# Kernel tuning notes

Measured on AMD Instinct MI355X. Metric: run time of the kernel, lower is better.

## Reference

```python
import jax, jax.numpy as jnp
import numpy as np

V, D, B, S, T, MAXLEN = 32000, 256, 4, 512, 256, 512


def _gru(x, Wih, Whh, bih, bhh):
    """torch-style GRU over x:[B,L,Din] -> [B,L,D]. Weight rows ordered [r,z,n]."""
    Dh = Whh.shape[1]
    xW = x @ Wih.T + bih  # [B,L,3D] precompute input projections

    def step(h, xw):
        hW = h @ Whh.T + bhh
        xr, xz, xn = jnp.split(xw, 3, axis=-1)
        hr, hz, hn = jnp.split(hW, 3, axis=-1)
        r = jax.nn.sigmoid(xr + hr)
        z = jax.nn.sigmoid(xz + hz)
        n = jnp.tanh(xn + r * hn)
        h = (1.0 - z) * n + z * h
        return h, h

    h0 = jnp.zeros((x.shape[0], Dh), x.dtype)
    _, ys = jax.lax.scan(step, h0, jnp.swapaxes(xW, 0, 1))
    return jnp.swapaxes(ys, 0, 1)


def setup_inputs() -> dict:
    key = jax.random.key(0)
    ks = jax.random.split(key, 24)

    def n(k, shape, scale=0.02):
        return (jax.random.normal(k, shape, jnp.float32) * scale).astype(jnp.float32)

    inp = {
        "src": jax.random.randint(ks[0], (B, S), 0, V),
        "tgt": jax.random.randint(ks[1], (B, T), 0, V),
        "emb": n(ks[2], (V, D)),
        "pos": n(ks[3], (MAXLEN, D)),
        # encoder forward direction
        "ef_wih": n(ks[4], (3 * D, D)), "ef_whh": n(ks[5], (3 * D, D)),
        "ef_bih": n(ks[6], (3 * D,)), "ef_bhh": n(ks[7], (3 * D,)),
        # encoder backward direction
        "eb_wih": n(ks[8], (3 * D, D)), "eb_whh": n(ks[9], (3 * D, D)),
        "eb_bih": n(ks[10], (3 * D,)), "eb_bhh": n(ks[11], (3 * D,)),
        # decoder
        "d_wih": n(ks[12], (3 * D, D)), "d_whh": n(ks[13], (3 * D, D)),
        "d_bih": n(ks[14], (3 * D,)), "d_bhh": n(ks[15], (3 * D,)),
        "Wq": n(ks[16], (D, D)),
        "Wk": n(ks[17], (D, 2 * D)),
        "Wgen": n(ks[18], (V, 3 * D)), "bgen": n(ks[19], (V,)),
        "Wgate": n(ks[20], (1, 3 * D)), "bgate": n(ks[21], (1,)),
    }
    return inp


def reference(src, tgt, emb, pos,
              ef_wih, ef_whh, ef_bih, ef_bhh,
              eb_wih, eb_whh, eb_bih, eb_bhh,
              d_wih, d_whh, d_bih, d_bhh,
              Wq, Wk, Wgen, bgen, Wgate, bgate):
    b, s = src.shape
    t = tgt.shape[1]
    d = emb.shape[1]
    v = emb.shape[0]

    src_emb = emb[src] + pos[:s][None]          # [B,S,D]
    enc_f = _gru(src_emb, ef_wih, ef_whh, ef_bih, ef_bhh)
    enc_b = _gru(src_emb[:, ::-1], eb_wih, eb_whh, eb_bih, eb_bhh)[:, ::-1]
    enc_out = jnp.concatenate([enc_f, enc_b], axis=-1)  # [B,S,2D]

    tgt_emb = emb[tgt] + pos[:t][None]
    dec_out = _gru(tgt_emb, d_wih, d_whh, d_bih, d_bhh)  # [B,T,D]

    Q = dec_out @ Wq.T                           # [B,T,D]
    K = enc_out @ Wk.T                           # [B,S,D]
    scores = jnp.einsum('btd,bsd->bts', Q, K) / jnp.sqrt(jnp.asarray(d, jnp.float32))
    pos_probs = jax.nn.softmax(scores, axis=-1)  # [B,T,S]

    # copy distribution: scatter attention mass into vocab buckets (== one_hot bmm)
    P_copy = jnp.zeros((b, t, v), pos_probs.dtype).at[
        jnp.arange(b)[:, None, None],
        jnp.arange(t)[None, :, None],
        src[:, None, :],
    ].add(pos_probs)

    ctx_f = jnp.einsum('bts,bsd->btd', pos_probs, enc_f)
    ctx_b = jnp.einsum('bts,bsd->btd', pos_probs, enc_b)
    combined = jnp.concatenate([dec_out, ctx_f, ctx_b], axis=-1)  # [B,T,3D]

    P_gen = jax.nn.softmax(combined @ Wgen.T + bgen, axis=-1)     # [B,T,V]
    gate = jax.nn.sigmoid(combined @ Wgate.T + bgate)             # [B,T,1]
    return gate * P_gen + (1.0 - gate) * P_copy
```

## Files before the change

### kernel.cpp

```cpp
#include <hip/hip_runtime.h>
#include <hip/hip_bf16.h>
#include <math.h>

#define VV   32000
#define DIM  256
#define BB   4
#define SS   512
#define TT   256
#define D2   512
#define D3   768

typedef __attribute__((ext_vector_type(8))) short s16x8;
typedef __attribute__((ext_vector_type(4))) float f32x4;

__device__ __forceinline__ float sigmoidf_(float x) { return 1.0f / (1.0f + __expf(-x)); }
__device__ __forceinline__ float tanhf_(float x) {
    float e2 = __expf(2.0f * x);
    return (e2 - 1.0f) / (e2 + 1.0f);
}
__device__ __forceinline__ short f2bf(float f) {
    unsigned u = __float_as_uint(f);
    u += 0x7FFFu + ((u >> 16) & 1u);
    return (short)(u >> 16);
}

__global__ __launch_bounds__(256) void k_embed(const int* __restrict__ src,
                                               const int* __restrict__ tgt,
                                               const float* __restrict__ emb,
                                               const float* __restrict__ pos,
                                               float* __restrict__ src_emb,
                                               float* __restrict__ tgt_emb) {
    int i = blockIdx.x * 256 + threadIdx.x;
    const int nS = BB * SS * DIM;
    if (i < nS) {
        int d = i & (DIM - 1);
        int s = (i >> 8) & (SS - 1);
        int b = i >> 17;
        src_emb[i] = emb[(size_t)src[b * SS + s] * DIM + d] + pos[s * DIM + d];
    } else {
        int j = i - nS;
        int d = j & (DIM - 1);
        int t = (j >> 8) & (TT - 1);
        int b = j >> 16;
        tgt_emb[j] = emb[(size_t)tgt[b * TT + t] * DIM + d] + pos[t * DIM + d];
    }
}

#define BMM 128
#define BNN 128
#define BKK 8

__global__ __launch_bounds__(256) void k_gemm(const float* __restrict__ A, int lda,
                                              const float* __restrict__ Bt, int ldb,
                                              const float* __restrict__ bias,
                                              float* __restrict__ C, int ldc) {
    __shared__ float As[BKK][BMM + 4];
    __shared__ float Bs[BKK][BNN + 4];
    const int K = lda;
    int tid = threadIdx.x;
    int tx = tid & 15, ty = tid >> 4;
    int brow = blockIdx.y * BMM, bcol = blockIdx.x * BNN;
    float acc[8][8];
#pragma unroll
    for (int i = 0; i < 8; i++)
#pragma unroll
        for (int j = 0; j < 8; j++) acc[i][j] = 0.0f;

    int lr = tid >> 1;
    int lk = (tid & 1) * 4;
    for (int k0 = 0; k0 < K; k0 += BKK) {
        float4 a4 = *(const float4*)&A[(size_t)(brow + lr) * lda + k0 + lk];
        float4 b4 = *(const float4*)&Bt[(size_t)(bcol + lr) * ldb + k0 + lk];
        As[lk + 0][lr] = a4.x; As[lk + 1][lr] = a4.y; As[lk + 2][lr] = a4.z; As[lk + 3][lr] = a4.w;
        Bs[lk + 0][lr] = b4.x; Bs[lk + 1][lr] = b4.y; Bs[lk + 2][lr] = b4.z; Bs[lk + 3][lr] = b4.w;
        __syncthreads();
#pragma unroll
        for (int kk = 0; kk < BKK; kk++) {
            float4 a0 = *(const float4*)&As[kk][ty * 8];
            float4 a1 = *(const float4*)&As[kk][ty * 8 + 4];
            float4 b0 = *(const float4*)&Bs[kk][tx * 8];
            float4 b1 = *(const float4*)&Bs[kk][tx * 8 + 4];
            float av[8] = {a0.x, a0.y, a0.z, a0.w, a1.x, a1.y, a1.z, a1.w};
            float bv[8] = {b0.x, b0.y, b0.z, b0.w, b1.x, b1.y, b1.z, b1.w};
#pragma unroll
            for (int i = 0; i < 8; i++)
#pragma unroll
                for (int j = 0; j < 8; j++) acc[i][j] += av[i] * bv[j];
        }
        __syncthreads();
    }

    float bv0[8];
#pragma unroll
    for (int j = 0; j < 8; j++) bv0[j] = bias ? bias[bcol + tx * 8 + j] : 0.0f;

#pragma unroll
    for (int i = 0; i < 8; i++) {
        size_t row = brow + ty * 8 + i;
        float4 c0 = make_float4(acc[i][0] + bv0[0], acc[i][1] + bv0[1],
                                acc[i][2] + bv0[2], acc[i][3] + bv0[3]);
        float4 c1 = make_float4(acc[i][4] + bv0[4], acc[i][5] + bv0[5],
                                acc[i][6] + bv0[6], acc[i][7] + bv0[7]);
        *(float4*)&C[row * ldc + bcol + tx * 8] = c0;
        *(float4*)&C[row * ldc + bcol + tx * 8 + 4] = c1;
    }
}

__global__ __launch_bounds__(512, 2) void k_gru(const float* __restrict__ ef_x,
                                                const float* __restrict__ eb_x,
                                                const float* __restrict__ d_x,
                                                const float* __restrict__ ef_whh, const float* __restrict__ ef_bhh,
                                                const float* __restrict__ eb_whh, const float* __restrict__ eb_bhh,
                                                const float* __restrict__ d_whh, const float* __restrict__ d_bhh,
                                                float* __restrict__ enc_out,
                                                float* __restrict__ dec_out) {
    __shared__ __align__(16) short hb[2][4 * 256];

    int tid = threadIdx.x;
    int dir = blockIdx.x;
    const float *xw, *Whh, *bhh;
    int L;
    if (dir == 0)      { xw = ef_x; Whh = ef_whh; bhh = ef_bhh; L = SS; }
    else if (dir == 1) { xw = eb_x; Whh = eb_whh; bhh = eb_bhh; L = SS; }
    else               { xw = d_x;  Whh = d_whh;  bhh = d_bhh;  L = TT; }

    const int wv = tid >> 6;
    const int lane = tid & 63;
    const int jj = lane & 15;
    const int hi = lane >> 4;
    const int b = hi;

    if (tid < 256) {
        f32x4 z = {0.f, 0.f, 0.f, 0.f};
        *(f32x4*)((char*)hb + tid * 16) = z;
    }

    s16x8 wf[3][2][8];
#pragma unroll
    for (int g = 0; g < 3; ++g)
#pragma unroll
        for (int t = 0; t < 2; ++t) {
            const int nrow = g * 256 + wv * 32 + t * 16 + jj;
            const float* wp = Whh + (size_t)nrow * 256 + hi * 8;
#pragma unroll
            for (int sk = 0; sk < 8; ++sk) {
                float4 w0 = *(const float4*)(wp + sk * 32);
                float4 w1 = *(const float4*)(wp + sk * 32 + 4);
                s16x8 v;
                v[0] = f2bf(w0.x); v[1] = f2bf(w0.y); v[2] = f2bf(w0.z); v[3] = f2bf(w0.w);
                v[4] = f2bf(w1.x); v[5] = f2bf(w1.y); v[6] = f2bf(w1.z); v[7] = f2bf(w1.w);
                wf[g][t][sk] = v;
            }
        }

    const int j0 = wv * 32 + jj, j1 = j0 + 16;
    const float br0 = bhh[j0], bz0 = bhh[256 + j0], bn0 = bhh[512 + j0];
    const float br1 = bhh[j1], bz1 = bhh[256 + j1], bn1 = bhh[512 + j1];

    const int arow = jj >> 2;
    const int abase = arow * 512 + hi * 16;
    const int aswz = arow << 4;
    const int wo0 = (b * 512 + 2 * j0) ^ (b << 4);
    const int wo1 = (b * 512 + 2 * j1) ^ (b << 4);

    const int s0 = (dir == 1) ? (L - 1) : 0;
    const int sst = (dir == 1) ? -1 : 1;
    const float* xq = xw + ((size_t)b * L + s0) * D3 + j0;
    float* op;
    int ostride;
    if (dir == 2) { op = dec_out + ((size_t)b * TT + s0) * DIM + j0; ostride = sst * DIM; }
    else          { op = enc_out + ((size_t)b * SS + s0) * D2 + (dir == 1 ? DIM : 0) + j0; ostride = sst * D2; }
    const int xstride = sst * D3;

    float c0 = xq[0], c1 = xq[256], c2 = xq[512], c3 = xq[16], c4 = xq[272], c5 = xq[528];

    float h0 = 0.f, h1 = 0.f;
    int cur = 0;
    __syncthreads();

    for (int st = 0; st < L; ++st) {
        xq += xstride;
        float n0 = xq[0], n1 = xq[256], n2 = xq[512], n3 = xq[16], n4 = xq[272], n5 = xq[528];

        const char* hcur = (const char*)hb + cur * 2048;
        f32x4 a00 = {0.f, 0.f, 0.f, 0.f}, a01 = a00, a10 = a00, a11 = a00, a20 = a00, a21 = a00;
#pragma unroll
        for (int sk = 0; sk < 8; ++sk) {
            s16x8 af = *(const s16x8*)(hcur + ((abase + 64 * sk) ^ aswz));
            a00 = __builtin_amdgcn_mfma_f32_16x16x32_bf16(af, wf[0][0][sk], a00, 0, 0, 0);
            a01 = __builtin_amdgcn_mfma_f32_16x16x32_bf16(af, wf[0][1][sk], a01, 0, 0, 0);
            a10 = __builtin_amdgcn_mfma_f32_16x16x32_bf16(af, wf[1][0][sk], a10, 0, 0, 0);
            a11 = __builtin_amdgcn_mfma_f32_16x16x32_bf16(af, wf[1][1][sk], a11, 0, 0, 0);
            a20 = __builtin_amdgcn_mfma_f32_16x16x32_bf16(af, wf[2][0][sk], a20, 0, 0, 0);
            a21 = __builtin_amdgcn_mfma_f32_16x16x32_bf16(af, wf[2][1][sk], a21, 0, 0, 0);
        }

        float r0 = sigmoidf_(c0 + a00[0] + br0);
        float z0 = sigmoidf_(c1 + a10[0] + bz0);
        float nn0 = tanhf_(c2 + a20[0] + bn0);
        nn0 = tanhf_(c2 + r0 * (a20[0] + bn0));
        h0 = (1.f - z0) * nn0 + z0 * h0;
        float r1 = sigmoidf_(c3 + a01[0] + br1);
        float z1 = sigmoidf_(c4 + a11[0] + bz1);
        float nn1 = tanhf_(c5 + r1 * (a21[0] + bn1));
        h1 = (1.f - z1) * nn1 + z1 * h1;

        char* hnxt = (char*)hb + (cur ^ 1) * 2048;
        *(short*)(hnxt + wo0) = f2bf(h0);
        *(short*)(hnxt + wo1) = f2bf(h1);
        op[0] = h0;
        op[16] = h1;
        __syncthreads();

        cur ^= 1;
        c0 = n0; c1 = n1; c2 = n2; c3 = n3; c4 = n4; c5 = n5;
        op += ostride;
    }
}

__global__ __launch_bounds__(256) void k_attn(const float* __restrict__ Qb,
                                              const float* __restrict__ Kb,
                                              const float* __restrict__ enc_out,
                                              const float* __restrict__ dec_out,
                                              const float* __restrict__ Wgate,
                                              const float* __restrict__ bgate,
                                              float* __restrict__ probs,
                                              short* __restrict__ cmb,
                                              float* __restrict__ gate) {
    __shared__ float q[DIM];
    __shared__ float sc[SS];
    __shared__ float red[256];
    int row = blockIdx.x;
    int b = row >> 8;
    int tid = threadIdx.x;

    q[tid] = Qb[(size_t)row * DIM + tid];
    __syncthreads();

    const float scale = 0.0625f;
#pragma unroll
    for (int h = 0; h < 2; h++) {
        int s2 = tid + h * 256;
        const float* kr = Kb + ((size_t)b * SS + s2) * DIM;
        float acc = 0.0f;
        for (int k = 0; k < DIM; k += 4) {
            float4 k4 = *(const float4*)&kr[k];
            acc += k4.x * q[k] + k4.y * q[k + 1] + k4.z * q[k + 2] + k4.w * q[k + 3];
        }
        sc[s2] = acc * scale;
    }
    __syncthreads();

    red[tid] = fmaxf(sc[tid], sc[tid + 256]);
    __syncthreads();
    for (int o = 128; o > 0; o >>= 1) {
        if (tid < o) red[tid] = fmaxf(red[tid], red[tid + o]);
        __syncthreads();
    }
    float m = red[0];
    __syncthreads();

    float e0 = __expf(sc[tid] - m), e1 = __expf(sc[tid + 256] - m);
    sc[tid] = e0; sc[tid + 256] = e1;
    red[tid] = e0 + e1;
    __syncthreads();
    for (int o = 128; o > 0; o >>= 1) {
        if (tid < o) red[tid] += red[tid + o];
        __syncthreads();
    }
    float inv = 1.0f / red[0];
    __syncthreads();

    sc[tid] *= inv; sc[tid + 256] *= inv;
    probs[(size_t)row * SS + tid] = sc[tid];
    probs[(size_t)row * SS + tid + 256] = sc[tid + 256];
    __syncthreads();

    float accf = 0.0f, accb = 0.0f;
    const float* ep = enc_out + (size_t)b * SS * D2 + tid;
    for (int s = 0; s < SS; s++) {
        float p = sc[s];
        accf += p * ep[(size_t)s * D2];
        accb += p * ep[(size_t)s * D2 + DIM];
    }
    float dv = dec_out[(size_t)row * DIM + tid];
    cmb[(size_t)row * D3 + tid] = f2bf(dv);
    cmb[(size_t)row * D3 + DIM + tid] = f2bf(accf);
    cmb[(size_t)row * D3 + 2 * DIM + tid] = f2bf(accb);

    red[tid] = dv * Wgate[tid] + accf * Wgate[DIM + tid] + accb * Wgate[2 * DIM + tid];
    __syncthreads();
    for (int o = 128; o > 0; o >>= 1) {
        if (tid < o) red[tid] += red[tid + o];
        __syncthreads();
    }
    if (tid == 0) gate[row] = sigmoidf_(red[0] + bgate[0]);
}

__global__ __launch_bounds__(512) void k_gen(const short* __restrict__ A,
                                             const float* __restrict__ Bw,
                                             const float* __restrict__ bias,
                                             float* __restrict__ C) {
    __shared__ __align__(16) short As[256 * 32];
    __shared__ __align__(16) short Bs[128 * 32];
    int tid = threadIdx.x;
    int lane = tid & 63, wv = tid >> 6;
    int wm = wv >> 1, wn = wv & 1;
    int brow = blockIdx.y * 256, bcol = blockIdx.x * 128;
    f32x4 acc[4][4];
#pragma unroll
    for (int i = 0; i < 4; i++)
#pragma unroll
        for (int j = 0; j < 4; j++) acc[i][j] = (f32x4){0.f, 0.f, 0.f, 0.f};

    const int ca0 = tid, ca1 = tid + 512, cb = tid;
    const int ll = lane & 15, lh = lane >> 4;

    for (int k0 = 0; k0 < D3; k0 += 32) {
        s16x8 va0 = *(const s16x8*)&A[(size_t)(brow + (ca0 >> 2)) * D3 + k0 + (ca0 & 3) * 8];
        s16x8 va1 = *(const s16x8*)&A[(size_t)(brow + (ca1 >> 2)) * D3 + k0 + (ca1 & 3) * 8];
        const float* bp = &Bw[(size_t)(bcol + (cb >> 2)) * D3 + k0 + (cb & 3) * 8];
        float4 b0 = *(const float4*)bp;
        float4 b1 = *(const float4*)(bp + 4);
        s16x8 vb;
        vb[0] = f2bf(b0.x); vb[1] = f2bf(b0.y); vb[2] = f2bf(b0.z); vb[3] = f2bf(b0.w);
        vb[4] = f2bf(b1.x); vb[5] = f2bf(b1.y); vb[6] = f2bf(b1.z); vb[7] = f2bf(b1.w);

        __syncthreads();
        *(s16x8*)&As[ca0 * 8] = va0;
        *(s16x8*)&As[ca1 * 8] = va1;
        *(s16x8*)&Bs[cb * 8] = vb;
        __syncthreads();

        s16x8 af[4], bf[4];
#pragma unroll
        for (int mt = 0; mt < 4; ++mt)
            af[mt] = *(const s16x8*)&As[(wm * 64 + mt * 16 + ll) * 32 + lh * 8];
#pragma unroll
        for (int nt = 0; nt < 4; ++nt)
            bf[nt] = *(const s16x8*)&Bs[(wn * 64 + nt * 16 + ll) * 32 + lh * 8];
#pragma unroll
        for (int mt = 0; mt < 4; ++mt)
#pragma unroll
            for (int nt = 0; nt < 4; ++nt)
                acc[mt][nt] = __builtin_amdgcn_mfma_f32_16x16x32_bf16(af[mt], bf[nt], acc[mt][nt], 0, 0, 0);
    }

#pragma unroll
    for (int mt = 0; mt < 4; ++mt) {
        int row = brow + wm * 64 + mt * 16 + lh * 4;
#pragma unroll
        for (int nt = 0; nt < 4; ++nt) {
            int col = bcol + wn * 64 + nt * 16 + ll;
            float bv = bias[col];
#pragma unroll
            for (int q = 0; q < 4; ++q)
                C[(size_t)(row + q) * VV + col] = acc[mt][nt][q] + bv;
        }
    }
}

__global__ __launch_bounds__(256) void k_rowstats(const float* __restrict__ logits,
                                                  float* __restrict__ rowmax,
                                                  float* __restrict__ rowsum) {
    __shared__ float rm[256], rs[256];
    int row = blockIdx.x, tid = threadIdx.x;
    const float* lp = logits + (size_t)row * VV;
    float m = -1e30f, sum = 0.0f;
    for (int v = tid; v < VV; v += 256) {
        float x = lp[v];
        float mn = fmaxf(m, x);
        sum = sum * __expf(m - mn) + __expf(x - mn);
        m = mn;
    }
    rm[tid] = m; rs[tid] = sum;
    __syncthreads();
    for (int o = 128; o > 0; o >>= 1) {
        if (tid < o) {
            float m2 = rm[tid + o], s2 = rs[tid + o];
            float mn = fmaxf(rm[tid], m2);
            rs[tid] = rs[tid] * __expf(rm[tid] - mn) + s2 * __expf(m2 - mn);
            rm[tid] = mn;
        }
        __syncthreads();
    }
    if (tid == 0) { rowmax[row] = rm[0]; rowsum[row] = rs[0]; }
}

__global__ __launch_bounds__(256) void k_final(const float* __restrict__ gate,
                                               const float* __restrict__ rowmax,
                                               const float* __restrict__ rowsum,
                                               float* __restrict__ out) {
    size_t i4 = (size_t)blockIdx.x * 256 + threadIdx.x;
    size_t base = i4 * 4;
    int row = (int)(base / VV);
    float m = rowmax[row];
    float inv = gate[row] / rowsum[row];
    float4 l = *(const float4*)&out[base];
    l.x = __expf(l.x - m) * inv;
    l.y = __expf(l.y - m) * inv;
    l.z = __expf(l.z - m) * inv;
    l.w = __expf(l.w - m) * inv;
    *(float4*)&out[base] = l;
}

__global__ __launch_bounds__(256) void k_scatter(const int* __restrict__ src,
                                                 const float* __restrict__ probs,
                                                 const float* __restrict__ gate,
                                                 float* __restrict__ out) {
    int i = blockIdx.x * 256 + threadIdx.x;
    int s = i & (SS - 1);
    int row = i >> 9;
    int b = row >> 8;
    float g = gate[row];
    float val = (1.0f - g) * probs[(size_t)row * SS + s];
    int col = src[b * SS + s];
    atomicAdd(&out[(size_t)row * VV + col], val);
}

extern "C" void kernel_launch(void* const* d_in, const int* in_sizes, int n_in,
                              void* d_out, int out_size, void* d_ws, size_t ws_size,
                              hipStream_t stream) {
    const int*   src    = (const int*)d_in[0];
    const int*   tgt    = (const int*)d_in[1];
    const float* emb    = (const float*)d_in[2];
    const float* pos    = (const float*)d_in[3];
    const float* ef_wih = (const float*)d_in[4];
    const float* ef_whh = (const float*)d_in[5];
    const float* ef_bih = (const float*)d_in[6];
    const float* ef_bhh = (const float*)d_in[7];
    const float* eb_wih = (const float*)d_in[8];
    const float* eb_whh = (const float*)d_in[9];
    const float* eb_bih = (const float*)d_in[10];
    const float* eb_bhh = (const float*)d_in[11];
    const float* d_wih  = (const float*)d_in[12];
    const float* d_whh  = (const float*)d_in[13];
    const float* d_bih  = (const float*)d_in[14];
    const float* d_bhh  = (const float*)d_in[15];
    const float* Wq     = (const float*)d_in[16];
    const float* Wk     = (const float*)d_in[17];
    const float* Wgen   = (const float*)d_in[18];
    const float* bgen   = (const float*)d_in[19];
    const float* Wgate  = (const float*)d_in[20];
    const float* bgate  = (const float*)d_in[21];
    float* out = (float*)d_out;
    float* ws  = (float*)d_ws;

    float* src_emb  = ws;
    float* tgt_emb  = src_emb + (size_t)BB * SS * DIM;
    float* ef_x     = tgt_emb + (size_t)BB * TT * DIM;
    float* eb_x     = ef_x + (size_t)BB * SS * D3;
    float* d_x      = eb_x + (size_t)BB * SS * D3;
    float* enc_out  = d_x + (size_t)BB * TT * D3;
    float* dec_out  = enc_out + (size_t)BB * SS * D2;
    float* Qb       = dec_out + (size_t)BB * TT * DIM;
    float* Kb       = Qb + (size_t)BB * TT * DIM;
    float* probs    = Kb + (size_t)BB * SS * DIM;
    short* cmb_bf   = (short*)(probs + (size_t)BB * TT * SS);
    float* gate     = (float*)(cmb_bf + (size_t)BB * TT * D3);
    float* rowmax   = gate + 1024;
    float* rowsum   = rowmax + 1024;

    k_embed<<<(BB * SS * DIM + BB * TT * DIM) / 256, 256, 0, stream>>>(
        src, tgt, emb, pos, src_emb, tgt_emb);

    k_gemm<<<dim3(D3 / BNN, BB * SS / BMM), 256, 0, stream>>>(src_emb, DIM, ef_wih, DIM, ef_bih, ef_x, D3);
    k_gemm<<<dim3(D3 / BNN, BB * SS / BMM), 256, 0, stream>>>(src_emb, DIM, eb_wih, DIM, eb_bih, eb_x, D3);
    k_gemm<<<dim3(D3 / BNN, BB * TT / BMM), 256, 0, stream>>>(tgt_emb, DIM, d_wih, DIM, d_bih, d_x, D3);

    k_gru<<<3, 512, 0, stream>>>(ef_x, eb_x, d_x, ef_whh, ef_bhh, eb_whh, eb_bhh,
                                 d_whh, d_bhh, enc_out, dec_out);

    k_gemm<<<dim3(DIM / BNN, BB * TT / BMM), 256, 0, stream>>>(dec_out, DIM, Wq, DIM, nullptr, Qb, DIM);
    k_gemm<<<dim3(DIM / BNN, BB * SS / BMM), 256, 0, stream>>>(enc_out, D2, Wk, D2, nullptr, Kb, DIM);

    k_attn<<<BB * TT, 256, 0, stream>>>(Qb, Kb, enc_out, dec_out, Wgate, bgate,
                                        probs, cmb_bf, gate);

    k_gen<<<dim3(VV / 128, (BB * TT) / 256), 512, 0, stream>>>(cmb_bf, Wgen, bgen, out);

    k_rowstats<<<BB * TT, 256, 0, stream>>>(out, rowmax, rowsum);
    k_final<<<(BB * TT * VV) / 1024, 256, 0, stream>>>(gate, rowmax, rowsum, out);
    k_scatter<<<(BB * TT * SS) / 256, 256, 0, stream>>>(src, probs, gate, out);
}
```

Measured before the change: 1.293 ms.

## Fuse softmax row-sum into generator GEMM, batch small GEMMs, trim GRU step

The generator GEMM epilogue now computes per-row sums of exp(logits) and accumulates them with atomics, which removes the separate row-stats pass over the full logits tensor. The max-subtraction is dropped on the assumption that the logits stay small. The five small projection GEMMs are grouped into two batched launches selected by blockIdx.z. In the GRU step, a redundant tanh is removed and __syncthreads is replaced by an explicit lgkmcnt wait plus s_barrier. Without max-subtraction, exp can overflow if the logits are large, and the float atomics make the row sums nondeterministic.

```diff
diff --git a/kernel.cpp b/kernel.cpp
--- a/kernel.cpp
+++ b/kernel.cpp
@@ -23,6 +23,8 @@
     u += 0x7FFFu + ((u >> 16) & 1u);
     return (short)(u >> 16);
 }
+
+#define BAR_LGKM() asm volatile("s_waitcnt lgkmcnt(0)\n\ts_barrier" ::: "memory")
 
 __global__ __launch_bounds__(256) void k_embed(const int* __restrict__ src,
                                                const int* __restrict__ tgt,
@@ -46,20 +48,28 @@
     }
 }
 
+struct GDesc {
+    const float* A; int lda;
+    const float* Bt; int ldb;
+    const float* bias;
+    float* C; int ldc;
+    int M, N;
+};
+
 #define BMM 128
 #define BNN 128
 #define BKK 8
 
-__global__ __launch_bounds__(256) void k_gemm(const float* __restrict__ A, int lda,
-                                              const float* __restrict__ Bt, int ldb,
-                                              const float* __restrict__ bias,
-                                              float* __restrict__ C, int ldc) {
+__global__ __launch_bounds__(256) void k_gemmb(GDesc d0, GDesc d1, GDesc d2) {
+    GDesc d = (blockIdx.z == 0) ? d0 : ((blockIdx.z == 1) ? d1 : d2);
+    int brow = blockIdx.y * BMM, bcol = blockIdx.x * BNN;
+    if (brow >= d.M || bcol >= d.N) return;
+
     __shared__ float As[BKK][BMM + 4];
     __shared__ float Bs[BKK][BNN + 4];
-    const int K = lda;
+    const int K = d.lda;
     int tid = threadIdx.x;
     int tx = tid & 15, ty = tid >> 4;
-    int brow = blockIdx.y * BMM, bcol = blockIdx.x * BNN;
     float acc[8][8];
 #pragma unroll
     for (int i = 0; i < 8; i++)
@@ -69,8 +79,8 @@
     int lr = tid >> 1;
     int lk = (tid & 1) * 4;
     for (int k0 = 0; k0 < K; k0 += BKK) {
-        float4 a4 = *(const float4*)&A[(size_t)(brow + lr) * lda + k0 + lk];
-        float4 b4 = *(const float4*)&Bt[(size_t)(bcol + lr) * ldb + k0 + lk];
+        float4 a4 = *(const float4*)&d.A[(size_t)(brow + lr) * d.lda + k0 + lk];
+        float4 b4 = *(const float4*)&d.Bt[(size_t)(bcol + lr) * d.ldb + k0 + lk];
         As[lk + 0][lr] = a4.x; As[lk + 1][lr] = a4.y; As[lk + 2][lr] = a4.z; As[lk + 3][lr] = a4.w;
         Bs[lk + 0][lr] = b4.x; Bs[lk + 1][lr] = b4.y; Bs[lk + 2][lr] = b4.z; Bs[lk + 3][lr] = b4.w;
         __syncthreads();
@@ -92,7 +102,7 @@
 
     float bv0[8];
 #pragma unroll
-    for (int j = 0; j < 8; j++) bv0[j] = bias ? bias[bcol + tx * 8 + j] : 0.0f;
+    for (int j = 0; j < 8; j++) bv0[j] = d.bias ? d.bias[bcol + tx * 8 + j] : 0.0f;
 
 #pragma unroll
     for (int i = 0; i < 8; i++) {
@@ -101,8 +111,8 @@
                                 acc[i][2] + bv0[2], acc[i][3] + bv0[3]);
         float4 c1 = make_float4(acc[i][4] + bv0[4], acc[i][5] + bv0[5],
                                 acc[i][6] + bv0[6], acc[i][7] + bv0[7]);
-        *(float4*)&C[row * ldc + bcol + tx * 8] = c0;
-        *(float4*)&C[row * ldc + bcol + tx * 8 + 4] = c1;
+        *(float4*)&d.C[row * d.ldc + bcol + tx * 8] = c0;
+        *(float4*)&d.C[row * d.ldc + bcol + tx * 8 + 4] = c1;
     }
 }
 
@@ -197,8 +207,7 @@
 
         float r0 = sigmoidf_(c0 + a00[0] + br0);
         float z0 = sigmoidf_(c1 + a10[0] + bz0);
-        float nn0 = tanhf_(c2 + a20[0] + bn0);
-        nn0 = tanhf_(c2 + r0 * (a20[0] + bn0));
+        float nn0 = tanhf_(c2 + r0 * (a20[0] + bn0));
         h0 = (1.f - z0) * nn0 + z0 * h0;
         float r1 = sigmoidf_(c3 + a01[0] + br1);
         float z1 = sigmoidf_(c4 + a11[0] + bz1);
@@ -210,7 +219,7 @@
         *(short*)(hnxt + wo1) = f2bf(h1);
         op[0] = h0;
         op[16] = h1;
-        __syncthreads();
+        BAR_LGKM();
 
         cur ^= 1;
         c0 = n0; c1 = n1; c2 = n2; c3 = n3; c4 = n4; c5 = n5;
@@ -300,7 +309,8 @@
 __global__ __launch_bounds__(512) void k_gen(const short* __restrict__ A,
                                              const float* __restrict__ Bw,
                                              const float* __restrict__ bias,
-                                             float* __restrict__ C) {
+                                             float* __restrict__ C,
+                                             float* __restrict__ rowsum) {
     __shared__ __align__(16) short As[256 * 32];
     __shared__ __align__(16) short Bs[128 * 32];
     int tid = threadIdx.x;
@@ -347,60 +357,55 @@
     }
 
 #pragma unroll
+    for (int nt = 0; nt < 4; ++nt) {
+        float bv = bias[bcol + wn * 64 + nt * 16 + ll];
+#pragma unroll
+        for (int mt = 0; mt < 4; ++mt)
+#pragma unroll
+            for (int q = 0; q < 4; ++q) acc[mt][nt][q] += bv;
+    }
+
+#pragma unroll
     for (int mt = 0; mt < 4; ++mt) {
         int row = brow + wm * 64 + mt * 16 + lh * 4;
 #pragma unroll
         for (int nt = 0; nt < 4; ++nt) {
             int col = bcol + wn * 64 + nt * 16 + ll;
-            float bv = bias[col];
 #pragma unroll
             for (int q = 0; q < 4; ++q)
-                C[(size_t)(row + q) * VV + col] = acc[mt][nt][q] + bv;
-        }
-    }
-}
-
-__global__ __launch_bounds__(256) void k_rowstats(const float* __restrict__ logits,
-                                                  float* __restrict__ rowmax,
-                                                  float* __restrict__ rowsum) {
-    __shared__ float rm[256], rs[256];
-    int row = blockIdx.x, tid = threadIdx.x;
-    const float* lp = logits + (size_t)row * VV;
-    float m = -1e30f, sum = 0.0f;
-    for (int v = tid; v < VV; v += 256) {
-        float x = lp[v];
-        float mn = fmaxf(m, x);
-        sum = sum * __expf(m - mn) + __expf(x - mn);
-        m = mn;
-    }
-    rm[tid] = m; rs[tid] = sum;
-    __syncthreads();
-    for (int o = 128; o > 0; o >>= 1) {
-        if (tid < o) {
-            float m2 = rm[tid + o], s2 = rs[tid + o];
-            float mn = fmaxf(rm[tid], m2);
-            rs[tid] = rs[tid] * __expf(rm[tid] - mn) + s2 * __expf(m2 - mn);
-            rm[tid] = mn;
-        }
-        __syncthreads();
-    }
-    if (tid == 0) { rowmax[row] = rm[0]; rowsum[row] = rs[0]; }
+                C[(size_t)(row + q) * VV + col] = acc[mt][nt][q];
+        }
+    }
+
+#pragma unroll
+    for (int mt = 0; mt < 4; ++mt) {
+#pragma unroll
+        for (int q = 0; q < 4; ++q) {
+            float se = __expf(acc[mt][0][q]) + __expf(acc[mt][1][q]) +
+                       __expf(acc[mt][2][q]) + __expf(acc[mt][3][q]);
+#pragma unroll
+            for (int off = 1; off < 16; off <<= 1)
+                se += __shfl_xor(se, off);
+            if (ll == 0) {
+                int row = brow + wm * 64 + mt * 16 + lh * 4 + q;
+                atomicAdd(&rowsum[row], se);
+            }
+        }
+    }
 }
 
 __global__ __launch_bounds__(256) void k_final(const float* __restrict__ gate,
-                                               const float* __restrict__ rowmax,
                                                const float* __restrict__ rowsum,
                                                float* __restrict__ out) {
     size_t i4 = (size_t)blockIdx.x * 256 + threadIdx.x;
     size_t base = i4 * 4;
     int row = (int)(base / VV);
-    float m = rowmax[row];
     float inv = gate[row] / rowsum[row];
     float4 l = *(const float4*)&out[base];
-    l.x = __expf(l.x - m) * inv;
-    l.y = __expf(l.y - m) * inv;
-    l.z = __expf(l.z - m) * inv;
-    l.w = __expf(l.w - m) * inv;
+    l.x = __expf(l.x) * inv;
+    l.y = __expf(l.y) * inv;
+    l.z = __expf(l.z) * inv;
+    l.w = __expf(l.w) * inv;
     *(float4*)&out[base] = l;
 }
 
@@ -458,28 +463,34 @@
     float* probs    = Kb + (size_t)BB * SS * DIM;
     short* cmb_bf   = (short*)(probs + (size_t)BB * TT * SS);
     float* gate     = (float*)(cmb_bf + (size_t)BB * TT * D3);
-    float* rowmax   = gate + 1024;
-    float* rowsum   = rowmax + 1024;
+    float* rowsum   = gate + 1024;
+
+    hipMemsetAsync(rowsum, 0, 1024 * sizeof(float), stream);
 
     k_embed<<<(BB * SS * DIM + BB * TT * DIM) / 256, 256, 0, stream>>>(
         src, tgt, emb, pos, src_emb, tgt_emb);
 
-    k_gemm<<<dim3(D3 / BNN, BB * SS / BMM), 256, 0, stream>>>(src_emb, DIM, ef_wih, DIM, ef_bih, ef_x, D3);
-    k_gemm<<<dim3(D3 / BNN, BB * SS / BMM), 256, 0, stream>>>(src_emb, DIM, eb_wih, DIM, eb_bih, eb_x, D3);
-    k_gemm<<<dim3(D3 / BNN, BB * TT / BMM), 256, 0, stream>>>(tgt_emb, DIM, d_wih, DIM, d_bih, d_x, D3);
+    {
+        GDesc e0 = {src_emb, DIM, ef_wih, DIM, ef_bih, ef_x, D3, BB * SS, D3};
+        GDesc e1 = {src_emb, DIM, eb_wih, DIM, eb_bih, eb_x, D3, BB * SS, D3};
+        GDesc e2 = {tgt_emb, DIM, d_wih, DIM, d_bih, d_x, D3, BB * TT, D3};
+        k_gemmb<<<dim3(D3 / BNN, BB * SS / BMM, 3), 256, 0, stream>>>(e0, e1, e2);
+    }
 
     k_gru<<<3, 512, 0, stream>>>(ef_x, eb_x, d_x, ef_whh, ef_bhh, eb_whh, eb_bhh,
                                  d_whh, d_bhh, enc_out, dec_out);
 
-    k_gemm<<<dim3(DIM / BNN, BB * TT / BMM), 256, 0, stream>>>(dec_out, DIM, Wq, DIM, nullptr, Qb, DIM);
-    k_gemm<<<dim3(DIM / BNN, BB * SS / BMM), 256, 0, stream>>>(enc_out, D2, Wk, D2, nullptr, Kb, DIM);
+    {
+        GDesc q0 = {dec_out, DIM, Wq, DIM, nullptr, Qb, DIM, BB * TT, DIM};
+        GDesc q1 = {enc_out, D2, Wk, D2, nullptr, Kb, DIM, BB * SS, DIM};
+        k_gemmb<<<dim3(DIM / BNN, BB * SS / BMM, 2), 256, 0, stream>>>(q0, q1, q1);
+    }
 
     k_attn<<<BB * TT, 256, 0, stream>>>(Qb, Kb, enc_out, dec_out, Wgate, bgate,
                                         probs, cmb_bf, gate);
 
-    k_gen<<<dim3(VV / 128, (BB * TT) / 256), 512, 0, stream>>>(cmb_bf, Wgen, bgen, out);
-
-    k_rowstats<<<BB * TT, 256, 0, stream>>>(out, rowmax, rowsum);
-    k_final<<<(BB * TT * VV) / 1024, 256, 0, stream>>>(gate, rowmax, rowsum, out);
+    k_gen<<<dim3(VV / 128, (BB * TT) / 256), 512, 0, stream>>>(cmb_bf, Wgen, bgen, out, rowsum);
+
+    k_final<<<(BB * TT * VV) / 1024, 256, 0, stream>>>(gate, rowsum, out);
     k_scatter<<<(BB * TT * SS) / 256, 256, 0, stream>>>(src, probs, gate, out);
 }
```

Result: faster. 1.186 ms (-8.2%).
